# Kernel optimization log

Hardware: AMD Instinct MI355X
Metric: run time of the kernel (lower is better)

## Reference

```python
import jax, jax.numpy as jnp
import numpy as np

DIM = 1536; HEADS = 12; HD = DIM // HEADS; FFN = 8960; EPS = 1e-6; T5 = 512
B = 1; F_ = 8; H_ = 18; W_ = 24; S = F_ * H_ * W_; L2 = T5 + 257


def _ln(x, w=None, b=None):
    m = x.mean(-1, keepdims=True)
    v = ((x - m) ** 2).mean(-1, keepdims=True)
    y = (x - m) * jax.lax.rsqrt(v + EPS)
    return y * w + b if w is not None else y


def _rms(x, w):
    return x * jax.lax.rsqrt(jnp.mean(x * x, -1, keepdims=True) + EPS) * w


def _gelu_tanh(z):
    return 0.5 * z * (1.0 + jnp.tanh(0.7978845608028654 * (z + 0.044715 * z * z * z)))


def _rope(x, F, H, W, ang):
    # x: [B,S,n,d]; ang: [1024, d//2] rotation angles (axial 3D RoPE)
    b, s, n, d = x.shape
    c = d // 2
    c1 = c // 3; c0 = c - 2 * c1  # split sizes [c0, c1, c1] over (F,H,W)
    fa = jnp.broadcast_to(ang[:F, :c0][:, None, None, :], (F, H, W, c0))
    ha = jnp.broadcast_to(ang[:H, c0:c0 + c1][None, :, None, :], (F, H, W, c1))
    wa = jnp.broadcast_to(ang[:W, c0 + c1:][None, None, :, :], (F, H, W, c1))
    th = jnp.concatenate([fa, ha, wa], -1).reshape(1, s, 1, c)
    cs, sn = jnp.cos(th), jnp.sin(th)
    xr = x.reshape(b, s, n, c, 2)
    re, im = xr[..., 0], xr[..., 1]
    return jnp.stack([re * cs - im * sn, re * sn + im * cs], -1).reshape(b, s, n, d)


def _attn(q, k, v):
    # dense softmax attention; [B,Lq,n,d] x [B,Lk,n,d]
    s = jnp.einsum('bqnd,bknd->bnqk', q, k) * (1.0 / np.sqrt(q.shape[-1]))
    p = jax.nn.softmax(s, axis=-1)
    return jnp.einsum('bnqk,bknd->bqnd', p, v)


def setup_inputs() -> dict:
    key = jax.random.key(0)
    ks = iter(jax.random.split(key, 64))
    g = lambda shp, sc=0.02: jax.random.normal(next(ks), shp, dtype=jnp.float32) * sc
    inp = {
        'x': jax.random.normal(next(ks), (B, S, DIM), dtype=jnp.float32),
        'e': jax.random.normal(next(ks), (B, 6, DIM), dtype=jnp.float32),
        'context': jax.random.normal(next(ks), (B, L2, DIM), dtype=jnp.float32),
        'freqs': jax.random.uniform(next(ks), (1024, HD // 2), dtype=jnp.float32),
        'modulation': g((1, 6, DIM)),
        'sa_qw': g((DIM, DIM)), 'sa_qb': jnp.zeros((DIM,), jnp.float32),
        'sa_kw': g((DIM, DIM)), 'sa_kb': jnp.zeros((DIM,), jnp.float32),
        'sa_vw': g((DIM, DIM)), 'sa_vb': jnp.zeros((DIM,), jnp.float32),
        'sa_ow': g((DIM, DIM)), 'sa_ob': jnp.zeros((DIM,), jnp.float32),
        'sa_nq': jnp.ones((DIM,), jnp.float32), 'sa_nk': jnp.ones((DIM,), jnp.float32),
        'norm3_w': jnp.ones((DIM,), jnp.float32), 'norm3_b': jnp.zeros((DIM,), jnp.float32),
        'ca_qw': g((DIM, DIM)), 'ca_qb': jnp.zeros((DIM,), jnp.float32),
        'ca_kw': g((DIM, DIM)), 'ca_kb': jnp.zeros((DIM,), jnp.float32),
        'ca_vw': g((DIM, DIM)), 'ca_vb': jnp.zeros((DIM,), jnp.float32),
        'ca_kiw': g((DIM, DIM)), 'ca_kib': jnp.zeros((DIM,), jnp.float32),
        'ca_viw': g((DIM, DIM)), 'ca_vib': jnp.zeros((DIM,), jnp.float32),
        'ca_ow': g((DIM, DIM)), 'ca_ob': jnp.zeros((DIM,), jnp.float32),
        'ca_nq': jnp.ones((DIM,), jnp.float32), 'ca_nk': jnp.ones((DIM,), jnp.float32),
        'ca_nki': jnp.ones((DIM,), jnp.float32),
        'ffn_w1': g((DIM, FFN)), 'ffn_b1': jnp.zeros((FFN,), jnp.float32),
        'ffn_w2': g((FFN, DIM)), 'ffn_b2': jnp.zeros((DIM,), jnp.float32),
        'F': F_, 'H': H_, 'W': W_,
    }
    return inp


def reference(x, e, context, freqs, modulation, sa_qw, sa_qb, sa_kw, sa_kb, sa_vw, sa_vb,
              sa_ow, sa_ob, sa_nq, sa_nk, norm3_w, norm3_b, ca_qw, ca_qb, ca_kw, ca_kb,
              ca_vw, ca_vb, ca_kiw, ca_kib, ca_viw, ca_vib, ca_ow, ca_ob, ca_nq, ca_nk,
              ca_nki, ffn_w1, ffn_b1, ffn_w2, ffn_b2, F, H, W):
    b, s, c = x.shape
    e6 = modulation + e                    # [B,6,C]
    e0, e1, e2, e3, e4, e5 = [e6[:, i:i + 1] for i in range(6)]

    # ---- self attention (with 3D RoPE, qk RMSNorm) ----
    xs = _ln(x) * (1.0 + e1) + e0
    q = _rms(xs @ sa_qw + sa_qb, sa_nq).reshape(b, s, HEADS, HD)
    k = _rms(xs @ sa_kw + sa_kb, sa_nk).reshape(b, s, HEADS, HD)
    v = (xs @ sa_vw + sa_vb).reshape(b, s, HEADS, HD)
    q = _rope(q, F, H, W, freqs)
    k = _rope(k, F, H, W, freqs)
    y = _attn(q, k, v).reshape(b, s, c) @ sa_ow + sa_ob
    x = x + y * e2

    # ---- i2v cross attention: text tokens (last T5) + image tokens (first L2-T5) ----
    xc = _ln(x, norm3_w, norm3_b)
    img_len = context.shape[1] - T5
    ctx_img = context[:, :img_len]
    ctx_txt = context[:, img_len:]
    q = _rms(xc @ ca_qw + ca_qb, ca_nq).reshape(b, s, HEADS, HD)
    k = _rms(ctx_txt @ ca_kw + ca_kb, ca_nk).reshape(b, T5, HEADS, HD)
    v = (ctx_txt @ ca_vw + ca_vb).reshape(b, T5, HEADS, HD)
    ki = _rms(ctx_img @ ca_kiw + ca_kib, ca_nki).reshape(b, img_len, HEADS, HD)
    vi = (ctx_img @ ca_viw + ca_vib).reshape(b, img_len, HEADS, HD)
    a = _attn(q, k, v) + _attn(q, ki, vi)
    x = x + a.reshape(b, s, c) @ ca_ow + ca_ob

    # ---- FFN with adaLN modulation ----
    z = _ln(x) * (1.0 + e4) + e3
    y = _gelu_tanh(z @ ffn_w1 + ffn_b1) @ ffn_w2 + ffn_b2
    x = x + y * e5
    return x
```

## Files before the change

### kernel.cpp

```cpp
#include <hip/hip_runtime.h>
#include <stdint.h>

#define DIM 1536
#define NHEADS 12
#define HD 128
#define FFN 8960
#define SQ 3456
#define T5 512
#define LCTX 769
#define IMG 257
#define IMGP 384
#define EPSL 1e-6f

typedef __bf16 bf16;
typedef __bf16 bf16x8 __attribute__((ext_vector_type(8)));
typedef float f32x4 __attribute__((ext_vector_type(4)));

__device__ inline bf16x8 zero_bf16x8() {
  bf16x8 v;
  for (int i = 0; i < 8; i++) v[i] = (bf16)0.0f;
  return v;
}

__device__ inline void glds16(const bf16* g, bf16* lds) {
  __builtin_amdgcn_global_load_lds(
      (const __attribute__((address_space(1))) void*)g,
      (__attribute__((address_space(3))) void*)lds, 16, 0, 0);
}


__global__ void prep_small_kernel(const float* __restrict__ modv, const float* __restrict__ e,
                                  float* __restrict__ e6f,
                                  const float* __restrict__ qb, const float* __restrict__ kb,
                                  const float* __restrict__ vb, float* __restrict__ qkvB,
                                  const float* __restrict__ ckb, const float* __restrict__ cvb,
                                  float* __restrict__ kvB,
                                  const float* __restrict__ kib, const float* __restrict__ vib,
                                  float* __restrict__ kivB) {
  int i = blockIdx.x * 256 + threadIdx.x;
  if (i < 6 * DIM) e6f[i] = modv[i] + e[i];
  if (i < DIM) {
    qkvB[i] = qb[i]; qkvB[i + DIM] = kb[i]; qkvB[i + 2 * DIM] = vb[i];
    kvB[i] = ckb[i]; kvB[i + DIM] = cvb[i];
    kivB[i] = kib[i]; kivB[i + DIM] = vib[i];
  }
}

__global__ void prep_ctx_kernel(const float* __restrict__ ctx, bf16* __restrict__ ctxt,
                                bf16* __restrict__ ctxi) {
  int i = blockIdx.x * 256 + threadIdx.x;
  if (i < T5 * DIM) ctxt[i] = (bf16)ctx[(size_t)IMG * DIM + i];
  if (i < IMGP * DIM) {
    int r = i / DIM;
    ctxi[i] = (r < IMG) ? (bf16)ctx[i] : (bf16)0.0f;
  }
}

__global__ void transpose_w3_kernel(const float* __restrict__ W0, const float* __restrict__ W1,
                                    const float* __restrict__ W2, bf16* __restrict__ Wt,
                                    int K, int N) {
  __shared__ float tile[32][33];
  const float* W = blockIdx.z == 0 ? W0 : (blockIdx.z == 1 ? W1 : W2);
  bf16* dst = Wt + (size_t)blockIdx.z * K * N;
  int n0 = blockIdx.x * 32, k0 = blockIdx.y * 32;
  int tx = threadIdx.x, ty = threadIdx.y;
  for (int i = ty; i < 32; i += 8)
    tile[i][tx] = W[(size_t)(k0 + i) * N + n0 + tx];
  __syncthreads();
  for (int i = ty; i < 32; i += 8)
    dst[(size_t)(n0 + i) * K + k0 + tx] = (bf16)tile[tx][i];
}

__device__ inline void block_reduce2(float& s1, float& s2) {
  __shared__ float buf[8];
  for (int off = 32; off; off >>= 1) {
    s1 += __shfl_down(s1, off, 64);
    s2 += __shfl_down(s2, off, 64);
  }
  int w = threadIdx.x >> 6;
  if ((threadIdx.x & 63) == 0) { buf[w] = s1; buf[w + 4] = s2; }
  __syncthreads();
  s1 = buf[0] + buf[1] + buf[2] + buf[3];
  s2 = buf[4] + buf[5] + buf[6] + buf[7];
  __syncthreads();
}

__global__ __launch_bounds__(256) void ln_mod_kernel(
    const float* __restrict__ X, const float* __restrict__ gamma,
    const float* __restrict__ beta, int plus_one, bf16* __restrict__ out) {
  int r = blockIdx.x;
  const float* xr = X + (size_t)r * DIM;
  float v[6], s = 0.f, s2 = 0.f;
  for (int i = 0; i < 6; i++) {
    v[i] = xr[threadIdx.x + i * 256];
    s += v[i]; s2 += v[i] * v[i];
  }
  block_reduce2(s, s2);
  float mean = s * (1.0f / DIM);
  float var = s2 * (1.0f / DIM) - mean * mean;
  float rstd = rsqrtf(var + EPSL);
  float add1 = plus_one ? 1.0f : 0.0f;
  for (int i = 0; i < 6; i++) {
    int c = threadIdx.x + i * 256;
    out[(size_t)r * DIM + c] = (bf16)(((v[i] - mean) * rstd) * (gamma[c] + add1) + beta[c]);
  }
}

__global__ __launch_bounds__(256) void rms_rope_multi_kernel(
    const float* __restrict__ X, int istride, int nsec,
    const float* __restrict__ nw0, const float* __restrict__ nw1,
    int mode0, int mode1, int mode2, float s0scale,
    const float* __restrict__ freqs,
    bf16* __restrict__ o0, bf16* __restrict__ o1, bf16* __restrict__ o2) {
  int sec = blockIdx.y;
  int r = blockIdx.x;
  const float* xr = X + (size_t)r * istride + sec * DIM;
  const float* nw = sec == 0 ? nw0 : nw1;
  bf16* out = (sec == 0 ? o0 : (sec == 1 ? o1 : o2)) + (size_t)r * DIM;
  int mode = sec == 0 ? mode0 : (sec == 1 ? mode1 : mode2);
  float v[6];
  for (int i = 0; i < 6; i++) v[i] = xr[threadIdx.x + i * 256];
  if (mode == 0) {
    for (int i = 0; i < 6; i++) out[threadIdx.x + i * 256] = (bf16)v[i];
    return;
  }
  float s2 = 0.f, dummy = 0.f;
  for (int i = 0; i < 6; i++) s2 += v[i] * v[i];
  block_reduce2(s2, dummy);
  float rms = rsqrtf(s2 * (1.0f / DIM) + EPSL);
  if (sec == 0) rms *= s0scale;
  if (mode == 1) {
    for (int i = 0; i < 6; i++) {
      int c = threadIdx.x + i * 256;
      out[c] = (bf16)(v[i] * rms * nw[c]);
    }
  } else {
    int f = r / (18 * 24), rem = r % (18 * 24), hh = rem / 24, ww = rem % 24;
    for (int i = 0; i < 3; i++) {
      int p = threadIdx.x + i * 256;
      int id = p & 63;
      int idx = id < 22 ? f : (id < 43 ? hh : ww);
      float th = freqs[idx * 64 + id];
      float cs = __cosf(th), sn = __sinf(th);
      float re = xr[2 * p] * rms * nw[2 * p];
      float im = xr[2 * p + 1] * rms * nw[2 * p + 1];
      out[2 * p]     = (bf16)(re * cs - im * sn);
      out[2 * p + 1] = (bf16)(re * sn + im * cs);
    }
  }
}

__global__ void ffn2_reduce_kernel(const float* __restrict__ p, const float* __restrict__ b2,
                                   const float* __restrict__ e5, const float* __restrict__ xcur,
                                   float* __restrict__ out) {
  int i = blockIdx.x * 256 + threadIdx.x;
  if (i >= SQ * DIM) return;
  int col = i % DIM;
  out[i] = xcur[i] + (p[i] + p[i + (size_t)SQ * DIM] + b2[col]) * e5[col];
}

template <int BM>
__global__ __launch_bounds__(256) void gemm_db_kernel(
    const bf16* __restrict__ A, const bf16* __restrict__ Wt,
    const float* __restrict__ bias, const float* __restrict__ scalev,
    const float* __restrict__ resid, float* __restrict__ outF,
    bf16* __restrict__ outB, int M, int N, int K, int gelu, int ksplit) {
  constexpr int MI = BM / 32;
  constexpr int NAW = BM / 64;
  __shared__ bf16 As[2][BM * 32];
  __shared__ bf16 Bs[2][128 * 32];
  int tid = threadIdx.x;
  int tm0 = blockIdx.y * BM, tn0 = blockIdx.x * 128;
  int lane = tid & 63, wave = tid >> 6;
  int quad = lane >> 4, l16 = lane & 15;
  int mbase = (wave >> 1) * (BM / 2), nbase = (wave & 1) * 64;
  int lrow = lane >> 2, lcol = (lane & 3) * 8;
  int klen = K / ksplit;
  int kbeg = blockIdx.z * klen;

  const bf16* aP[NAW];
  const bf16* bP[2];
#pragma unroll
  for (int j = 0; j < NAW; j++) {
    int c = wave * NAW + j;
    aP[j] = A + (size_t)(tm0 + c * 16 + lrow) * K + kbeg + lcol;
  }
#pragma unroll
  for (int j = 0; j < 2; j++) {
    int c = wave * 2 + j;
    bP[j] = Wt + (size_t)(tn0 + c * 16 + lrow) * K + kbeg + lcol;
  }

  f32x4 acc[MI][4];
#pragma unroll
  for (int mi = 0; mi < MI; mi++)
    for (int ni = 0; ni < 4; ni++)
      for (int rr = 0; rr < 4; rr++) acc[mi][ni][rr] = 0.0f;

  auto stage = [&](int buf) {
#pragma unroll
    for (int j = 0; j < NAW; j++) {
      glds16(aP[j], &As[buf][(wave * NAW + j) * 512]);
      aP[j] += 32;
    }
#pragma unroll
    for (int j = 0; j < 2; j++) {
      glds16(bP[j], &Bs[buf][(wave * 2 + j) * 512]);
      bP[j] += 32;
    }
  };

  int niter = klen / 32;
  stage(0);
  int cur = 0;
  for (int it = 0; it < niter; it++) {
    __syncthreads();
    if (it + 1 < niter) stage(cur ^ 1);
    bf16x8 af[MI], bfr[4];
#pragma unroll
    for (int mi = 0; mi < MI; mi++)
      af[mi] = *(bf16x8*)&As[cur][(mbase + mi * 16 + l16) * 32 + quad * 8];
#pragma unroll
    for (int ni = 0; ni < 4; ni++)
      bfr[ni] = *(bf16x8*)&Bs[cur][(nbase + ni * 16 + l16) * 32 + quad * 8];
#pragma unroll
    for (int mi = 0; mi < MI; mi++)
#pragma unroll
      for (int ni = 0; ni < 4; ni++)
        acc[mi][ni] = __builtin_amdgcn_mfma_f32_16x16x32_bf16(af[mi], bfr[ni], acc[mi][ni], 0, 0, 0);
    cur ^= 1;
  }

  if (ksplit > 1) {
    float* po = outF + (size_t)blockIdx.z * M * N;
#pragma unroll
    for (int mi = 0; mi < MI; mi++) {
      int rbase = tm0 + mbase + mi * 16 + quad * 4;
#pragma unroll
      for (int ni = 0; ni < 4; ni++) {
        int col = tn0 + nbase + ni * 16 + l16;
        for (int rr = 0; rr < 4; rr++)
          po[(size_t)(rbase + rr) * N + col] = acc[mi][ni][rr];
      }
    }
    return;
  }

#pragma unroll
  for (int mi = 0; mi < MI; mi++) {
    int rbase = tm0 + mbase + mi * 16 + quad * 4;
#pragma unroll
    for (int ni = 0; ni < 4; ni++) {
      int col = tn0 + nbase + ni * 16 + l16;
      float b = bias ? bias[col] : 0.0f;
      float sc = scalev ? scalev[col] : 1.0f;
      for (int rr = 0; rr < 4; rr++) {
        int row = rbase + rr;
        float t = acc[mi][ni][rr] + b;
        if (gelu) {
          float z = t;
          float u = 0.7978845608028654f * (z + 0.044715f * z * z * z);
          t = z / (1.0f + __expf(-2.0f * u));
        }
        t *= sc;
        size_t idx = (size_t)row * N + col;
        if (resid) t += resid[idx];
        if (outF) outF[idx] = t;
        else outB[idx] = (bf16)t;
      }
    }
  }
}

__global__ __launch_bounds__(256) void attn_kernel(
    const bf16* __restrict__ Q, const bf16* __restrict__ Kb, const bf16* __restrict__ Vb,
    const bf16* __restrict__ Kb2, const bf16* __restrict__ Vb2,
    float* __restrict__ Opart, float* __restrict__ mlb,
    int L, int kchunk, int zsplit1, int Lsec, int kchunk2) {
  __shared__ __align__(16) bf16 Ks[64][136];
  __shared__ __align__(16) bf16 Vts[128][72];
  __shared__ __align__(16) bf16 Ps[4][16][72];

  int nwg = gridDim.x * gridDim.y * gridDim.z;
  int flat = blockIdx.x + gridDim.x * (blockIdx.y + gridDim.y * blockIdx.z);
  if ((nwg & 7) == 0) flat = (flat & 7) * (nwg >> 3) + (flat >> 3);
  int bx = flat % gridDim.x;
  int rest = flat / gridDim.x;
  int hb = rest % gridDim.y;
  int bz = rest / gridDim.y;

  int tid = threadIdx.x;
  int q0 = bx * 64;
  int sec = bz >= zsplit1;
  int bzl = sec ? bz - zsplit1 : bz;
  const bf16* Kp = sec ? Kb2 : Kb;
  const bf16* Vp = sec ? Vb2 : Vb;
  int Lv = sec ? Lsec : L;
  int kch = sec ? kchunk2 : kchunk;
  int kbeg = bzl * kch;
  int kend = min(Lv, kbeg + kch);
  int klen = kend - kbeg;
  int zabs = bz;
  int lane = tid & 63, wave = tid >> 6;
  int quad = lane >> 4, l16 = lane & 15;
  int qrow = q0 + wave * 16 + l16;

  bf16x8 qf[4];
#pragma unroll
  for (int c = 0; c < 4; c++)
    qf[c] = *(const bf16x8*)(Q + (size_t)qrow * DIM + hb * HD + c * 32 + quad * 8);

  bf16x8 onesv;
#pragma unroll
  for (int i = 0; i < 8; i++) onesv[i] = (bf16)1.0f;

  f32x4 o[8];
#pragma unroll
  for (int ff = 0; ff < 8; ff++)
    for (int rr = 0; rr < 4; rr++) o[ff][rr] = 0.0f;
  float m_i[4], l_i[4];
#pragma unroll
  for (int r = 0; r < 4; r++) { m_i[r] = -1e30f; l_i[r] = 0.0f; }

  int srow = tid >> 2, scolc = tid & 3;
  int vdg = tid >> 5, vl = (tid >> 1) & 15, vh = tid & 1;
  int nt = (klen + 63) / 64;
  int tail = (klen & 63) != 0;

  const bf16* kp0 = Kp + (size_t)(kbeg + srow) * DIM + hb * HD + scolc * 8;
  const bf16* vp0 = Vp + (size_t)(kbeg + vh * 32 + vl) * DIM + hb * HD + vdg * 16;
  char* vwp = (char*)&Vts[0][0] + vdg * (16 * 144) + (4 * vl + 2 * vh) * 2;

  bf16x8 kreg[4], vreg[4];
  if (srow < klen) {
#pragma unroll
    for (int c = 0; c < 4; c++) kreg[c] = *(const bf16x8*)(kp0 + c * 32);
  } else {
#pragma unroll
    for (int c = 0; c < 4; c++) kreg[c] = zero_bf16x8();
  }
  if (vh * 32 + vl < klen) {
    vreg[0] = *(const bf16x8*)vp0;
    vreg[1] = *(const bf16x8*)(vp0 + 8);
  } else { vreg[0] = zero_bf16x8(); vreg[1] = zero_bf16x8(); }
  if (vh * 32 + vl + 16 < klen) {
    vreg[2] = *(const bf16x8*)(vp0 + 16 * DIM);
    vreg[3] = *(const bf16x8*)(vp0 + 16 * DIM + 8);
  } else { vreg[2] = zero_bf16x8(); vreg[3] = zero_bf16x8(); }

  for (int kt = 0; kt < nt; kt++) {
    __syncthreads();
#pragma unroll
    for (int c = 0; c < 4; c++)
      *(bf16x8*)&Ks[srow][scolc * 8 + c * 32] = kreg[c];
    {
      union U8 { bf16x8 v; uint32_t w[4]; };
      U8 a0, a1, b0, b1;
      a0.v = vreg[0]; a1.v = vreg[1]; b0.v = vreg[2]; b1.v = vreg[3];
#pragma unroll
      for (int j = 0; j < 16; j++) {
        uint32_t w0 = (j < 8) ? a0.w[(j & 7) >> 1] : a1.w[(j & 7) >> 1];
        uint32_t w1 = (j < 8) ? b0.w[(j & 7) >> 1] : b1.w[(j & 7) >> 1];
        uint32_t pk = (j & 1) ? ((w0 >> 16) | (w1 & 0xFFFF0000u))
                              : ((w0 & 0xFFFFu) | (w1 << 16));
        *(uint32_t*)(vwp + j * 144) = pk;
      }
    }
    if (kt + 1 < nt) {
      int kb64 = (kt + 1) * 64;
      const bf16* kp = kp0 + (size_t)(kt + 1) * 64 * DIM;
      const bf16* vp = vp0 + (size_t)(kt + 1) * 64 * DIM;
      if (kb64 + srow < klen) {
#pragma unroll
        for (int c = 0; c < 4; c++) kreg[c] = *(const bf16x8*)(kp + c * 32);
      } else {
#pragma unroll
        for (int c = 0; c < 4; c++) kreg[c] = zero_bf16x8();
      }
      if (kb64 + vh * 32 + vl < klen) {
        vreg[0] = *(const bf16x8*)vp;
        vreg[1] = *(const bf16x8*)(vp + 8);
      } else { vreg[0] = zero_bf16x8(); vreg[1] = zero_bf16x8(); }
      if (kb64 + vh * 32 + vl + 16 < klen) {
        vreg[2] = *(const bf16x8*)(vp + 16 * DIM);
        vreg[3] = *(const bf16x8*)(vp + 16 * DIM + 8);
      } else { vreg[2] = zero_bf16x8(); vreg[3] = zero_bf16x8(); }
    }
    __syncthreads();

    f32x4 sfr[4];
    __builtin_amdgcn_s_setprio(1);
#pragma unroll
    for (int nf = 0; nf < 4; nf++) {
      f32x4 a;
      for (int rr = 0; rr < 4; rr++) a[rr] = 0.0f;
#pragma unroll
      for (int c = 0; c < 4; c++) {
        bf16x8 kf = *(bf16x8*)&Ks[nf * 16 + l16][c * 32 + quad * 8];
        a = __builtin_amdgcn_mfma_f32_16x16x32_bf16(qf[c], kf, a, 0, 0, 0);
      }
      sfr[nf] = a;
    }
    __builtin_amdgcn_s_setprio(0);

    if (tail && kt == nt - 1) {
#pragma unroll
      for (int nf = 0; nf < 4; nf++) {
        int colg = kt * 64 + nf * 16 + l16;
        bool valid = colg < klen;
#pragma unroll
        for (int r = 0; r < 4; r++)
          sfr[nf][r] = valid ? sfr[nf][r] : -1e30f;
      }
    }

    float lmax[4];
#pragma unroll
    for (int r = 0; r < 4; r++)
      lmax[r] = fmaxf(fmaxf(sfr[0][r], sfr[1][r]), fmaxf(sfr[2][r], sfr[3][r]));
    int ok = (lmax[0] <= m_i[0] + 11.54f) & (lmax[1] <= m_i[1] + 11.54f) &
             (lmax[2] <= m_i[2] + 11.54f) & (lmax[3] <= m_i[3] + 11.54f);
    if (!__all(ok)) {
#pragma unroll
      for (int r = 0; r < 4; r++) {
        float t = lmax[r];
#pragma unroll
        for (int off = 1; off < 16; off <<= 1) t = fmaxf(t, __shfl_xor(t, off, 64));
        float mnew = fmaxf(m_i[r], t);
        float alpha = exp2f(m_i[r] - mnew);
        m_i[r] = mnew;
        l_i[r] *= alpha;
#pragma unroll
        for (int ff = 0; ff < 8; ff++) o[ff][r] *= alpha;
      }
    }

#pragma unroll
    for (int r = 0; r < 4; r++) {
      union { bf16 b[4]; unsigned long long u; } pk;
      pk.b[0] = (bf16)exp2f(sfr[0][r] - m_i[r]);
      pk.b[1] = (bf16)exp2f(sfr[1][r] - m_i[r]);
      pk.b[2] = (bf16)exp2f(sfr[2][r] - m_i[r]);
      pk.b[3] = (bf16)exp2f(sfr[3][r] - m_i[r]);
      *(unsigned long long*)((char*)&Ps[wave][quad * 4 + r][0] + l16 * 8) = pk.u;
    }
    bf16x8 pf[2];
#pragma unroll
    for (int ks = 0; ks < 2; ks++)
      pf[ks] = *(bf16x8*)&Ps[wave][l16][ks * 32 + quad * 8];

    __builtin_amdgcn_s_setprio(1);
    f32x4 ld;
    for (int rr = 0; rr < 4; rr++) ld[rr] = 0.0f;
    ld = __builtin_amdgcn_mfma_f32_16x16x32_bf16(pf[0], onesv, ld, 0, 0, 0);
    ld = __builtin_amdgcn_mfma_f32_16x16x32_bf16(pf[1], onesv, ld, 0, 0, 0);
#pragma unroll
    for (int ff = 0; ff < 8; ff++) {
#pragma unroll
      for (int ks = 0; ks < 2; ks++) {
        bf16x8 vf = *(bf16x8*)&Vts[ff * 16 + l16][ks * 32 + quad * 8];
        o[ff] = __builtin_amdgcn_mfma_f32_16x16x32_bf16(pf[ks], vf, o[ff], 0, 0, 0);
      }
    }
    __builtin_amdgcn_s_setprio(0);
#pragma unroll
    for (int r = 0; r < 4; r++) l_i[r] += ld[r];
  }

  float* po = Opart + (size_t)zabs * SQ * DIM;
#pragma unroll
  for (int r = 0; r < 4; r++) {
    float inv = 1.0f / l_i[r];
#pragma unroll
    for (int ff = 0; ff < 8; ff++) o[ff][r] *= inv;
  }
#pragma unroll
  for (int ff = 0; ff < 8; ff++) {
#pragma unroll
    for (int r = 0; r < 4; r++) {
      int row = q0 + wave * 16 + quad * 4 + r;
      int col = hb * HD + ff * 16 + l16;
      po[(size_t)row * DIM + col] = o[ff][r];
    }
  }
  if (l16 == 0) {
#pragma unroll
    for (int r = 0; r < 4; r++) {
      int row = q0 + wave * 16 + quad * 4 + r;
      size_t mi = (((size_t)zabs * NHEADS + hb) * SQ + row) * 2;
      mlb[mi] = m_i[r];
      mlb[mi + 1] = l_i[r];
    }
  }
}

__global__ __launch_bounds__(256) void attn_combine_kernel(
    const float* __restrict__ Op, const float* __restrict__ mlb,
    bf16* __restrict__ out, int nmerge, int addslot) {
  int row = blockIdx.x;
  __shared__ float wsh[3 * NHEADS];
  int t = threadIdx.x;
  if (t < NHEADS) {
    float m[3], l[3];
    for (int z = 0; z < 3; z++) {
      if (z < nmerge) {
        size_t b = (((size_t)z * NHEADS + t) * SQ + row) * 2;
        m[z] = mlb[b]; l[z] = mlb[b + 1];
      } else {
        m[z] = -1e30f; l[z] = 0.0f;
      }
    }
    float M = fmaxf(m[0], fmaxf(m[1], m[2]));
    float w0 = l[0] * exp2f(m[0] - M);
    float w1 = l[1] * exp2f(m[1] - M);
    float w2 = l[2] * exp2f(m[2] - M);
    float inv = 1.0f / (w0 + w1 + w2);
    wsh[t] = w0 * inv;
    wsh[NHEADS + t] = w1 * inv;
    wsh[2 * NHEADS + t] = w2 * inv;
  }
  __syncthreads();
#pragma unroll
  for (int i = 0; i < 6; i++) {
    int c = t + i * 256;
    int h = c >> 7;
    float acc = wsh[h] * Op[((size_t)0 * SQ + row) * DIM + c];
    if (nmerge > 1) acc += wsh[NHEADS + h] * Op[((size_t)1 * SQ + row) * DIM + c];
    if (nmerge > 2) acc += wsh[2 * NHEADS + h] * Op[((size_t)2 * SQ + row) * DIM + c];
    if (addslot >= 0) acc += Op[((size_t)addslot * SQ + row) * DIM + c];
    out[(size_t)row * DIM + c] = (bf16)acc;
  }
}


extern "C" void kernel_launch(void* const* d_in, const int* in_sizes, int n_in,
                              void* d_out, int out_size, void* d_ws, size_t ws_size,
                              hipStream_t stream) {
  const float* x      = (const float*)d_in[0];
  const float* e      = (const float*)d_in[1];
  const float* ctx    = (const float*)d_in[2];
  const float* freqs  = (const float*)d_in[3];
  const float* modv   = (const float*)d_in[4];
  const float* sa_qw  = (const float*)d_in[5];
  const float* sa_qb  = (const float*)d_in[6];
  const float* sa_kw  = (const float*)d_in[7];
  const float* sa_kb  = (const float*)d_in[8];
  const float* sa_vw  = (const float*)d_in[9];
  const float* sa_vb  = (const float*)d_in[10];
  const float* sa_ow  = (const float*)d_in[11];
  const float* sa_ob  = (const float*)d_in[12];
  const float* sa_nq  = (const float*)d_in[13];
  const float* sa_nk  = (const float*)d_in[14];
  const float* norm3w = (const float*)d_in[15];
  const float* norm3b = (const float*)d_in[16];
  const float* ca_qw  = (const float*)d_in[17];
  const float* ca_qb  = (const float*)d_in[18];
  const float* ca_kw  = (const float*)d_in[19];
  const float* ca_kb  = (const float*)d_in[20];
  const float* ca_vw  = (const float*)d_in[21];
  const float* ca_vb  = (const float*)d_in[22];
  const float* ca_kiw = (const float*)d_in[23];
  const float* ca_kib = (const float*)d_in[24];
  const float* ca_viw = (const float*)d_in[25];
  const float* ca_vib = (const float*)d_in[26];
  const float* ca_ow  = (const float*)d_in[27];
  const float* ca_ob  = (const float*)d_in[28];
  const float* ca_nq  = (const float*)d_in[29];
  const float* ca_nk  = (const float*)d_in[30];
  const float* ca_nki = (const float*)d_in[31];
  const float* ffn_w1 = (const float*)d_in[32];
  const float* ffn_b1 = (const float*)d_in[33];
  const float* ffn_w2 = (const float*)d_in[34];
  const float* ffn_b2 = (const float*)d_in[35];

  char* ws = (char*)d_ws;
  size_t off = 0;
  auto alloc = [&](size_t bytes) -> void* {
    void* p = ws + off;
    off += (bytes + 255) & ~(size_t)255;
    return p;
  };
  float* e6f   = (float*)alloc((size_t)6 * DIM * 4);
  bf16* act_bf = (bf16*)alloc((size_t)SQ * DIM * 2);
  bf16* q_bf   = (bf16*)alloc((size_t)SQ * DIM * 2);
  bf16* k_bf   = (bf16*)alloc((size_t)SQ * DIM * 2);
  bf16* v_bf   = (bf16*)alloc((size_t)SQ * DIM * 2);
  char* big0   = (char*)alloc((size_t)SQ * 3 * DIM * 4);
  float* xcur  = (float*)alloc((size_t)SQ * DIM * 4);
  bf16* wbig   = (bf16*)alloc((size_t)FFN * DIM * 2);
  bf16* wsm    = (bf16*)alloc((size_t)3 * DIM * DIM * 2);
  bf16* ctxt_bf = (bf16*)alloc((size_t)T5 * DIM * 2);
  bf16* ctxi_bf = (bf16*)alloc((size_t)IMGP * DIM * 2);
  float* ctxkvF = (float*)alloc((size_t)T5 * 2 * DIM * 4);
  float* ctxkivF = (float*)alloc((size_t)IMGP * 2 * DIM * 4);
  bf16* kt_bf  = (bf16*)alloc((size_t)T5 * DIM * 2);
  bf16* vt_bf  = (bf16*)alloc((size_t)T5 * DIM * 2);
  bf16* ki_bf  = (bf16*)alloc((size_t)IMGP * DIM * 2);
  bf16* vi_bf  = (bf16*)alloc((size_t)IMGP * DIM * 2);
  float* qkvB  = (float*)alloc((size_t)3 * DIM * 4);
  float* kvB   = (float*)alloc((size_t)2 * DIM * 4);
  float* kivB  = (float*)alloc((size_t)2 * DIM * 4);
  float* mlbuf = (float*)alloc((size_t)3 * NHEADS * SQ * 2 * 4);

  float* qkvF = (float*)big0;
  float* projf = (float*)big0;
  float* opart = (float*)big0;
  bf16* y1 = (bf16*)big0;
  float* pbuf = (float*)act_bf;

  const float* e0 = e6f;
  const float* e1 = e6f + DIM;
  const float* e2 = e6f + 2 * DIM;
  const float* e3 = e6f + 3 * DIM;
  const float* e4 = e6f + 4 * DIM;
  const float* e5 = e6f + 5 * DIM;

  const float SCL2 = 0.12751744f;

  dim3 tblk(32, 8);

  prep_small_kernel<<<(6 * DIM + 255) / 256, 256, 0, stream>>>(
      modv, e, e6f, sa_qb, sa_kb, sa_vb, qkvB, ca_kb, ca_vb, kvB, ca_kib, ca_vib, kivB);

  ln_mod_kernel<<<SQ, 256, 0, stream>>>(x, e1, e0, 1, act_bf);

  transpose_w3_kernel<<<dim3(48, 48, 3), tblk, 0, stream>>>(sa_qw, sa_kw, sa_vw, wbig, DIM, DIM);
  gemm_db_kernel<128><<<dim3(3 * DIM / 128, SQ / 128), 256, 0, stream>>>(
      act_bf, wbig, qkvB, nullptr, nullptr, qkvF, nullptr, SQ, 3 * DIM, DIM, 0, 1);
  rms_rope_multi_kernel<<<dim3(SQ, 3), 256, 0, stream>>>(
      qkvF, 3 * DIM, 3, sa_nq, sa_nk, 2, 2, 0, SCL2, freqs, q_bf, k_bf, v_bf);

  attn_kernel<<<dim3(SQ / 64, NHEADS, 3), 256, 0, stream>>>(
      q_bf, k_bf, v_bf, k_bf, v_bf, opart, mlbuf, SQ, SQ / 3, 3, SQ, SQ / 3);
  attn_combine_kernel<<<SQ, 256, 0, stream>>>(opart, mlbuf, act_bf, 3, -1);

  transpose_w3_kernel<<<dim3(48, 48, 1), tblk, 0, stream>>>(sa_ow, nullptr, nullptr, wsm, DIM, DIM);
  gemm_db_kernel<64><<<dim3(DIM / 128, SQ / 64), 256, 0, stream>>>(
      act_bf, wsm, sa_ob, e2, x, xcur, nullptr, SQ, DIM, DIM, 0, 1);

  ln_mod_kernel<<<SQ, 256, 0, stream>>>(xcur, norm3w, norm3b, 0, act_bf);

  transpose_w3_kernel<<<dim3(48, 48, 1), tblk, 0, stream>>>(ca_qw, nullptr, nullptr, wsm, DIM, DIM);
  gemm_db_kernel<64><<<dim3(DIM / 128, SQ / 64), 256, 0, stream>>>(
      act_bf, wsm, ca_qb, nullptr, nullptr, projf, nullptr, SQ, DIM, DIM, 0, 1);
  rms_rope_multi_kernel<<<dim3(SQ, 1), 256, 0, stream>>>(
      projf, DIM, 1, ca_nq, nullptr, 1, 0, 0, SCL2, freqs, q_bf, nullptr, nullptr);

  prep_ctx_kernel<<<(T5 * DIM + 255) / 256, 256, 0, stream>>>(ctx, ctxt_bf, ctxi_bf);

  transpose_w3_kernel<<<dim3(48, 48, 2), tblk, 0, stream>>>(ca_kw, ca_vw, nullptr, wsm, DIM, DIM);
  gemm_db_kernel<64><<<dim3(2 * DIM / 128, T5 / 64), 256, 0, stream>>>(
      ctxt_bf, wsm, kvB, nullptr, nullptr, ctxkvF, nullptr, T5, 2 * DIM, DIM, 0, 1);
  rms_rope_multi_kernel<<<dim3(T5, 2), 256, 0, stream>>>(
      ctxkvF, 2 * DIM, 2, ca_nk, nullptr, 1, 0, 0, 1.0f, freqs, kt_bf, vt_bf, nullptr);

  transpose_w3_kernel<<<dim3(48, 48, 2), tblk, 0, stream>>>(ca_kiw, ca_viw, nullptr, wsm, DIM, DIM);
  gemm_db_kernel<64><<<dim3(2 * DIM / 128, IMGP / 64), 256, 0, stream>>>(
      ctxi_bf, wsm, kivB, nullptr, nullptr, ctxkivF, nullptr, IMGP, 2 * DIM, DIM, 0, 1);
  rms_rope_multi_kernel<<<dim3(IMGP, 2), 256, 0, stream>>>(
      ctxkivF, 2 * DIM, 2, ca_nki, nullptr, 1, 0, 0, 1.0f, freqs, ki_bf, vi_bf, nullptr);

  attn_kernel<<<dim3(SQ / 64, NHEADS, 3), 256, 0, stream>>>(
      q_bf, kt_bf, vt_bf, ki_bf, vi_bf, opart, mlbuf, T5, T5 / 2, 2, IMG, IMG);
  attn_combine_kernel<<<SQ, 256, 0, stream>>>(opart, mlbuf, act_bf, 2, 2);

  transpose_w3_kernel<<<dim3(48, 48, 1), tblk, 0, stream>>>(ca_ow, nullptr, nullptr, wsm, DIM, DIM);
  gemm_db_kernel<64><<<dim3(DIM / 128, SQ / 64), 256, 0, stream>>>(
      act_bf, wsm, ca_ob, nullptr, xcur, xcur, nullptr, SQ, DIM, DIM, 0, 1);

  ln_mod_kernel<<<SQ, 256, 0, stream>>>(xcur, e4, e3, 1, act_bf);

  transpose_w3_kernel<<<dim3(FFN / 32, 48, 1), tblk, 0, stream>>>(ffn_w1, nullptr, nullptr, wbig, DIM, FFN);
  gemm_db_kernel<128><<<dim3(FFN / 128, SQ / 128), 256, 0, stream>>>(
      act_bf, wbig, ffn_b1, nullptr, nullptr, nullptr, y1, SQ, FFN, DIM, 1, 1);

  transpose_w3_kernel<<<dim3(48, FFN / 32, 1), tblk, 0, stream>>>(ffn_w2, nullptr, nullptr, wbig, FFN, DIM);
  gemm_db_kernel<128><<<dim3(DIM / 128, SQ / 128, 2), 256, 0, stream>>>(
      y1, wbig, nullptr, nullptr, nullptr, pbuf, nullptr, SQ, DIM, FFN, 0, 2);
  ffn2_reduce_kernel<<<(SQ * DIM + 255) / 256, 256, 0, stream>>>(
      pbuf, ffn_b2, e5, xcur, (float*)d_out);
}
```

Before: 1.221 ms.

## Double attention query tile to 128 rows with 512-thread blocks sharing K/V tiles

The attention kernel now processes 128 query rows per workgroup with 8 waves instead of 64 rows with 4. Each K/V tile staged in shared memory is therefore reused by twice as many queries, and the per-thread global load and transpose work is halved. The XCD remapping is generalized to grids not divisible by 8, and exp2f is replaced by the hardware exp2 builtin. Fewer workgroups may reduce occupancy or balance, and the 512-thread launch bound may force register pressure.

```diff
diff --git a/kernel.cpp b/kernel.cpp
--- a/kernel.cpp
+++ b/kernel.cpp
@@ -20,6 +20,14 @@
   bf16x8 v;
   for (int i = 0; i < 8; i++) v[i] = (bf16)0.0f;
   return v;
+}
+
+__device__ inline float fexp2(float x) {
+#if __has_builtin(__builtin_amdgcn_exp2f)
+  return __builtin_amdgcn_exp2f(x);
+#else
+  return exp2f(x);
+#endif
 }
 
 __device__ inline void glds16(const bf16* g, bf16* lds) {
@@ -272,25 +280,28 @@
   }
 }
 
-__global__ __launch_bounds__(256) void attn_kernel(
+__global__ __launch_bounds__(512, 4) void attn_kernel(
     const bf16* __restrict__ Q, const bf16* __restrict__ Kb, const bf16* __restrict__ Vb,
     const bf16* __restrict__ Kb2, const bf16* __restrict__ Vb2,
     float* __restrict__ Opart, float* __restrict__ mlb,
     int L, int kchunk, int zsplit1, int Lsec, int kchunk2) {
   __shared__ __align__(16) bf16 Ks[64][136];
   __shared__ __align__(16) bf16 Vts[128][72];
-  __shared__ __align__(16) bf16 Ps[4][16][72];
+  __shared__ __align__(16) bf16 Ps[8][16][72];
 
   int nwg = gridDim.x * gridDim.y * gridDim.z;
   int flat = blockIdx.x + gridDim.x * (blockIdx.y + gridDim.y * blockIdx.z);
-  if ((nwg & 7) == 0) flat = (flat & 7) * (nwg >> 3) + (flat >> 3);
+  {
+    int xcd = flat & 7, g8 = flat >> 3, qq = nwg >> 3, r8 = nwg & 7;
+    flat = (xcd < r8 ? xcd * (qq + 1) : r8 * (qq + 1) + (xcd - r8) * qq) + g8;
+  }
   int bx = flat % gridDim.x;
   int rest = flat / gridDim.x;
   int hb = rest % gridDim.y;
   int bz = rest / gridDim.y;
 
   int tid = threadIdx.x;
-  int q0 = bx * 64;
+  int q0 = bx * 128;
   int sec = bz >= zsplit1;
   int bzl = sec ? bz - zsplit1 : bz;
   const bf16* Kp = sec ? Kb2 : Kb;
@@ -322,45 +333,34 @@
 #pragma unroll
   for (int r = 0; r < 4; r++) { m_i[r] = -1e30f; l_i[r] = 0.0f; }
 
-  int srow = tid >> 2, scolc = tid & 3;
-  int vdg = tid >> 5, vl = (tid >> 1) & 15, vh = tid & 1;
+  int srow = tid >> 3, scolc = tid & 7;
+  int low6 = tid & 63;
+  int vh = low6 & 1, vd2 = (low6 >> 1) & 1, vl = low6 >> 2;
   int nt = (klen + 63) / 64;
   int tail = (klen & 63) != 0;
 
   const bf16* kp0 = Kp + (size_t)(kbeg + srow) * DIM + hb * HD + scolc * 8;
-  const bf16* vp0 = Vp + (size_t)(kbeg + vh * 32 + vl) * DIM + hb * HD + vdg * 16;
-  char* vwp = (char*)&Vts[0][0] + vdg * (16 * 144) + (4 * vl + 2 * vh) * 2;
-
-  bf16x8 kreg[4], vreg[4];
+  const bf16* vp0 = Vp + (size_t)(kbeg + vh * 32 + vl) * DIM + hb * HD + wave * 16 + vd2 * 8;
+  char* vwp = (char*)&Vts[0][0] + (wave * 16 + vd2 * 8) * 144 + (4 * vl + 2 * vh) * 2;
+
+  bf16x8 kreg[2], va, vb;
   if (srow < klen) {
-#pragma unroll
-    for (int c = 0; c < 4; c++) kreg[c] = *(const bf16x8*)(kp0 + c * 32);
-  } else {
-#pragma unroll
-    for (int c = 0; c < 4; c++) kreg[c] = zero_bf16x8();
-  }
-  if (vh * 32 + vl < klen) {
-    vreg[0] = *(const bf16x8*)vp0;
-    vreg[1] = *(const bf16x8*)(vp0 + 8);
-  } else { vreg[0] = zero_bf16x8(); vreg[1] = zero_bf16x8(); }
-  if (vh * 32 + vl + 16 < klen) {
-    vreg[2] = *(const bf16x8*)(vp0 + 16 * DIM);
-    vreg[3] = *(const bf16x8*)(vp0 + 16 * DIM + 8);
-  } else { vreg[2] = zero_bf16x8(); vreg[3] = zero_bf16x8(); }
+    kreg[0] = *(const bf16x8*)kp0;
+    kreg[1] = *(const bf16x8*)(kp0 + 64);
+  } else { kreg[0] = zero_bf16x8(); kreg[1] = zero_bf16x8(); }
+  va = (vh * 32 + vl < klen) ? *(const bf16x8*)vp0 : zero_bf16x8();
+  vb = (vh * 32 + vl + 16 < klen) ? *(const bf16x8*)(vp0 + 16 * DIM) : zero_bf16x8();
 
   for (int kt = 0; kt < nt; kt++) {
     __syncthreads();
-#pragma unroll
-    for (int c = 0; c < 4; c++)
-      *(bf16x8*)&Ks[srow][scolc * 8 + c * 32] = kreg[c];
+    *(bf16x8*)&Ks[srow][scolc * 8] = kreg[0];
+    *(bf16x8*)&Ks[srow][scolc * 8 + 64] = kreg[1];
     {
       union U8 { bf16x8 v; uint32_t w[4]; };
-      U8 a0, a1, b0, b1;
-      a0.v = vreg[0]; a1.v = vreg[1]; b0.v = vreg[2]; b1.v = vreg[3];
-#pragma unroll
-      for (int j = 0; j < 16; j++) {
-        uint32_t w0 = (j < 8) ? a0.w[(j & 7) >> 1] : a1.w[(j & 7) >> 1];
-        uint32_t w1 = (j < 8) ? b0.w[(j & 7) >> 1] : b1.w[(j & 7) >> 1];
+      U8 ua, ub; ua.v = va; ub.v = vb;
+#pragma unroll
+      for (int j = 0; j < 8; j++) {
+        uint32_t w0 = ua.w[j >> 1], w1 = ub.w[j >> 1];
         uint32_t pk = (j & 1) ? ((w0 >> 16) | (w1 & 0xFFFF0000u))
                               : ((w0 & 0xFFFFu) | (w1 << 16));
         *(uint32_t*)(vwp + j * 144) = pk;
@@ -371,20 +371,11 @@
       const bf16* kp = kp0 + (size_t)(kt + 1) * 64 * DIM;
       const bf16* vp = vp0 + (size_t)(kt + 1) * 64 * DIM;
       if (kb64 + srow < klen) {
-#pragma unroll
-        for (int c = 0; c < 4; c++) kreg[c] = *(const bf16x8*)(kp + c * 32);
-      } else {
-#pragma unroll
-        for (int c = 0; c < 4; c++) kreg[c] = zero_bf16x8();
-      }
-      if (kb64 + vh * 32 + vl < klen) {
-        vreg[0] = *(const bf16x8*)vp;
-        vreg[1] = *(const bf16x8*)(vp + 8);
-      } else { vreg[0] = zero_bf16x8(); vreg[1] = zero_bf16x8(); }
-      if (kb64 + vh * 32 + vl + 16 < klen) {
-        vreg[2] = *(const bf16x8*)(vp + 16 * DIM);
-        vreg[3] = *(const bf16x8*)(vp + 16 * DIM + 8);
-      } else { vreg[2] = zero_bf16x8(); vreg[3] = zero_bf16x8(); }
+        kreg[0] = *(const bf16x8*)kp;
+        kreg[1] = *(const bf16x8*)(kp + 64);
+      } else { kreg[0] = zero_bf16x8(); kreg[1] = zero_bf16x8(); }
+      va = (kb64 + vh * 32 + vl < klen) ? *(const bf16x8*)vp : zero_bf16x8();
+      vb = (kb64 + vh * 32 + vl + 16 < klen) ? *(const bf16x8*)(vp + 16 * DIM) : zero_bf16x8();
     }
     __syncthreads();
 
@@ -427,7 +418,7 @@
 #pragma unroll
         for (int off = 1; off < 16; off <<= 1) t = fmaxf(t, __shfl_xor(t, off, 64));
         float mnew = fmaxf(m_i[r], t);
-        float alpha = exp2f(m_i[r] - mnew);
+        float alpha = fexp2(m_i[r] - mnew);
         m_i[r] = mnew;
         l_i[r] *= alpha;
 #pragma unroll
@@ -438,10 +429,10 @@
 #pragma unroll
     for (int r = 0; r < 4; r++) {
       union { bf16 b[4]; unsigned long long u; } pk;
-      pk.b[0] = (bf16)exp2f(sfr[0][r] - m_i[r]);
-      pk.b[1] = (bf16)exp2f(sfr[1][r] - m_i[r]);
-      pk.b[2] = (bf16)exp2f(sfr[2][r] - m_i[r]);
-      pk.b[3] = (bf16)exp2f(sfr[3][r] - m_i[r]);
+      pk.b[0] = (bf16)fexp2(sfr[0][r] - m_i[r]);
+      pk.b[1] = (bf16)fexp2(sfr[1][r] - m_i[r]);
+      pk.b[2] = (bf16)fexp2(sfr[2][r] - m_i[r]);
+      pk.b[3] = (bf16)fexp2(sfr[3][r] - m_i[r]);
       *(unsigned long long*)((char*)&Ps[wave][quad * 4 + r][0] + l16 * 8) = pk.u;
     }
     bf16x8 pf[2];
@@ -511,9 +502,9 @@
       }
     }
     float M = fmaxf(m[0], fmaxf(m[1], m[2]));
-    float w0 = l[0] * exp2f(m[0] - M);
-    float w1 = l[1] * exp2f(m[1] - M);
-    float w2 = l[2] * exp2f(m[2] - M);
+    float w0 = l[0] * fexp2(m[0] - M);
+    float w1 = l[1] * fexp2(m[1] - M);
+    float w2 = l[2] * fexp2(m[2] - M);
     float inv = 1.0f / (w0 + w1 + w2);
     wsh[t] = w0 * inv;
     wsh[NHEADS + t] = w1 * inv;
@@ -630,7 +621,7 @@
   rms_rope_multi_kernel<<<dim3(SQ, 3), 256, 0, stream>>>(
       qkvF, 3 * DIM, 3, sa_nq, sa_nk, 2, 2, 0, SCL2, freqs, q_bf, k_bf, v_bf);
 
-  attn_kernel<<<dim3(SQ / 64, NHEADS, 3), 256, 0, stream>>>(
+  attn_kernel<<<dim3(SQ / 128, NHEADS, 3), 512, 0, stream>>>(
       q_bf, k_bf, v_bf, k_bf, v_bf, opart, mlbuf, SQ, SQ / 3, 3, SQ, SQ / 3);
   attn_combine_kernel<<<SQ, 256, 0, stream>>>(opart, mlbuf, act_bf, 3, -1);
 
@@ -660,7 +651,7 @@
   rms_rope_multi_kernel<<<dim3(IMGP, 2), 256, 0, stream>>>(
       ctxkivF, 2 * DIM, 2, ca_nki, nullptr, 1, 0, 0, 1.0f, freqs, ki_bf, vi_bf, nullptr);
 
-  attn_kernel<<<dim3(SQ / 64, NHEADS, 3), 256, 0, stream>>>(
+  attn_kernel<<<dim3(SQ / 128, NHEADS, 3), 512, 0, stream>>>(
       q_bf, kt_bf, vt_bf, ki_bf, vi_bf, opart, mlbuf, T5, T5 / 2, 2, IMG, IMG);
   attn_combine_kernel<<<SQ, 256, 0, stream>>>(opart, mlbuf, act_bf, 2, 2);
 
```

Measured after the change: 1.133 ms. 7.2% less time.
